# Kernel optimization log

Measured on AMD Instinct MI355X. Metric: run time of the kernel, lower is better.

## Reference

```python
import jax, jax.numpy as jnp
import numpy as np

B, T, D = 16, 512, 256          # batch, seq_len, d_model (= num features = num graph nodes N)
H, MC, K, DE, DH = 4, 4, 3, 10, 128
GS, SS, AS = 4, 6, 4            # global/sector/asset regime states
TAU = 0.5
STEPS = 3                       # diffusion steps
HID = max(64, D)
DEC_H = max(64, D // 2)


def setup_inputs() -> dict:
    key = jax.random.key(0)
    ks = iter(jax.random.split(key, 64))

    def nrm(shape, s=0.02):
        return (s * jax.random.normal(next(ks), shape)).astype(jnp.float32)

    z = lambda *s: jnp.zeros(s, jnp.float32)
    o = lambda *s: jnp.ones(s, jnp.float32)
    p = dict(
        x=jax.random.normal(next(ks), (B, T, D), dtype=jnp.float32),
        # hierarchical regime controller
        gW1=nrm((D, HID)), gb1=z(HID), g_ln_w=o(HID), g_ln_b=z(HID),
        gW2=nrm((HID, GS)), gb2=z(GS),
        sW1=nrm((D, HID)), sb1=z(HID), sW2=nrm((HID, D * SS)), sb2=z(D * SS),
        aW1=nrm((D, HID)), ab1=z(HID), aW2=nrm((HID, D * AS)), ab2=z(D * AS),
        global_prior=z(GS), sector_prior=z(SS), asset_prior=z(AS),
        g2f=nrm((GS, D)),
        sector_emb=jax.random.normal(next(ks), (SS, D), dtype=jnp.float32),
        asset_emb=jax.random.normal(next(ks), (AS, D), dtype=jnp.float32),
        # bidirectional temporal scan (BI-Mamba stand-in)
        decay_f=nrm((D,), 1.0), decay_b=nrm((D,), 1.0),
        tW=nrm((D, D)), tb=z(D),
        # Bayesian MAGAC + diffusion graph prior
        psi=nrm((H, D, DE), 0.1), log_sigma=jnp.full((H,), -2.0, jnp.float32),
        step_logits=jnp.linspace(-1.0, 0.5, STEPS).astype(jnp.float32),
        noise_scale=jnp.full((STEPS,), 0.05, jnp.float32),
        Wk=nrm((K + 1, T, DH)),
        mean_w=nrm((DH,)), mean_b=z(), lv_w=nrm((DH,)), lv_b=z(),
        # risk-aware decoder
        dW1=nrm((D, DEC_H)), db1=z(DEC_H), d_ln_w=o(DEC_H), d_ln_b=z(DEC_H),
        mW=nrm((DEC_H,)), mb=z(), lvW=nrm((DEC_H,)), lvb=z(),
        cW=nrm((DEC_H,)), cb=z(),
    )
    return p


def _ln(h, w, b):
    m = h.mean(-1, keepdims=True)
    v = h.var(-1, keepdims=True)  # biased, matches torch LayerNorm
    return (h - m) / jnp.sqrt(v + 1e-5) * w + b


def _gelu(h):
    return jax.nn.gelu(h, approximate=False)


def _gumbel_softmax(k, logits):
    u = jax.random.uniform(k, logits.shape, minval=1e-6, maxval=1.0 - 1e-6)
    g = -jnp.log(-jnp.log(u))
    return jax.nn.softmax((logits + g) / TAU, axis=-1)


def _fwd(x, gW1, gb1, g_ln_w, g_ln_b, gW2, gb2, sW1, sb1, sW2, sb2,
         aW1, ab1, aW2, ab2, global_prior, sector_prior, asset_prior,
         g2f, sector_emb, asset_emb, decay_f, decay_b, tW, tb,
         psi, log_sigma, step_logits, noise_scale, Wk,
         mean_w, mean_b, lv_w, lv_b,
         dW1, db1, d_ln_w, d_ln_b, mW, mb, lvW, lvb, cW, cb):
    rk = jax.random.key(42)
    k_g, k_s, k_a, k_eps, k_diff = jax.random.split(rk, 5)

    # ---- hierarchical regime controller ----
    seq_mean = x.mean(1)                               # (B, D)
    diff_summary = (x[:, 1:] - x[:, :-1]).mean(1)      # (B, D)
    g_logits = _gelu(_ln(seq_mean @ gW1 + gb1, g_ln_w, g_ln_b)) @ gW2 + gb2
    s_logits = (_gelu(seq_mean @ sW1 + sb1) @ sW2 + sb2).reshape(B, D, SS)
    a_logits = (_gelu(diff_summary @ aW1 + ab1) @ aW2 + ab2).reshape(B, D, AS)
    g_probs = _gumbel_softmax(k_g, g_logits)
    s_probs = _gumbel_softmax(k_s, s_logits)
    a_probs = _gumbel_softmax(k_a, a_logits)
    global_gate = g_probs @ g2f                                   # (B, D)
    # diagonal of einsum('bfs,sd->bfd') == einsum('bfs,sf->bf')
    sector_gate = jnp.einsum('bfs,sf->bf', s_probs, sector_emb)
    asset_gate = jnp.einsum('bfs,sf->bf', a_probs, asset_emb)
    feature_gate = jax.nn.sigmoid(global_gate + sector_gate + asset_gate)
    gated_x = x * feature_gate[:, None, :]

    # ---- bidirectional temporal EMA scan (BI-Mamba stand-in) ----
    af = jax.nn.sigmoid(decay_f)
    abk = jax.nn.sigmoid(decay_b)
    xs = gated_x.transpose(1, 0, 2)                    # (T, B, D)

    def ema(a):
        def step(h, xt):
            h = a * h + (1.0 - a) * xt
            return h, h
        return step

    _, hf = jax.lax.scan(ema(af), jnp.zeros_like(xs[0]), xs)
    _, hb = jax.lax.scan(ema(abk), jnp.zeros_like(xs[0]), xs[::-1])
    temporal = (hf + hb[::-1]).transpose(1, 0, 2) @ tW + tb       # (B, T, D)
    node_major = temporal.transpose(0, 2, 1)                      # (B, N=D, T)

    # ---- Bayesian adjacency sampling (MC samples per head) ----
    logits = jnp.einsum('hne,hme->hnm', psi, psi) / jnp.sqrt(jnp.float32(DE))
    sigma = jnp.exp(log_sigma)                                    # (H,)
    eps = jax.random.normal(k_eps, (MC, H, D, D))
    A = jax.nn.softmax(logits[None] + sigma[None, :, None, None] * eps, axis=-1)

    # ---- diffusion refinement guided by regime features ----
    ctx = feature_gate.mean(0)
    ctx = ctx / (jnp.linalg.norm(ctx) + 1e-6)
    outer = ctx[:, None] * ctx[None, :]
    outer = outer / jnp.maximum(outer.sum(-1, keepdims=True), 1e-6)
    dkeys = jax.random.split(k_diff, STEPS)
    for s in range(STEPS):                             # fixed small loop, vectorized over (MC,H)
        alpha = jax.nn.sigmoid(step_logits[s])
        noise = noise_scale[s] * jax.random.normal(dkeys[s], A.shape)
        A = alpha * A + (1.0 - alpha) * outer + noise
        A = 0.5 * (A + jnp.swapaxes(A, -1, -2))
        A = jax.nn.softmax(A, axis=-1)

    # ---- K-hop graph conv, averaged over MC samples and heads ----
    Z = jnp.einsum('bnt,td->bnd', node_major, Wk[0])[None, None]  # hop 0
    P = jnp.broadcast_to(node_major, (MC, H, B, D, T))
    for k in range(1, K + 1):
        P = jnp.einsum('mhnp,mhbpt->mhbnt', A, P)
        Z = Z + jnp.einsum('mhbnt,td->mhbnd', P, Wk[k])
    Z = Z.mean((0, 1))                                            # (B, N, DH)
    graph_mean = Z @ mean_w + mean_b                              # (B, N)
    graph_logvar = Z @ lv_w + lv_b                                # (B, N)

    # ---- risk-aware decoder ----
    feat = _ln(_gelu(graph_mean @ dW1 + db1), d_ln_w, d_ln_b)     # (B, DEC_H)
    mean = feat @ mW + mb
    dec_logvar = feat @ lvW + lvb
    _cvar = jax.nn.sigmoid(feat @ cW + cb)  # auxiliary head (not in returned output)
    var = jnp.exp(dec_logvar) + jnp.exp(graph_logvar).sum(1)
    log_var = jnp.log(var)
    return jnp.stack([mean, log_var], axis=-1)                    # (B, 2)


def reference(x, gW1, gb1, g_ln_w, g_ln_b, gW2, gb2, sW1, sb1, sW2, sb2,
              aW1, ab1, aW2, ab2, global_prior, sector_prior, asset_prior,
              g2f, sector_emb, asset_emb, decay_f, decay_b, tW, tb,
              psi, log_sigma, step_logits, noise_scale, Wk,
              mean_w, mean_b, lv_w, lv_b,
              dW1, db1, d_ln_w, d_ln_b, mW, mb, lvW, lvb, cW, cb):
    return _fwd(x, gW1, gb1, g_ln_w, g_ln_b, gW2, gb2, sW1, sb1, sW2, sb2,
                aW1, ab1, aW2, ab2, global_prior, sector_prior, asset_prior,
                g2f, sector_emb, asset_emb, decay_f, decay_b, tW, tb,
                psi, log_sigma, step_logits, noise_scale, Wk,
                mean_w, mean_b, lv_w, lv_b,
                dW1, db1, d_ln_w, d_ln_b, mW, mb, lvW, lvb, cW, cb)
```

## Files before the change

kernel.cpp:

```cpp
#include <hip/hip_runtime.h>
#include <stdint.h>

#define PARTITIONABLE 1

namespace {

struct TFPair { uint32_t a, b; };

__host__ __device__ constexpr uint32_t rotl32(uint32_t x, int d) {
  return (x << d) | (x >> (32 - d));
}

__host__ __device__ constexpr TFPair tf2x32(uint32_t k0, uint32_t k1,
                                            uint32_t x0, uint32_t x1) {
  uint32_t k2 = k0 ^ k1 ^ 0x1BD11BDAu;
  x0 += k0; x1 += k1;
  x0 += x1; x1 = rotl32(x1, 13); x1 ^= x0;
  x0 += x1; x1 = rotl32(x1, 15); x1 ^= x0;
  x0 += x1; x1 = rotl32(x1, 26); x1 ^= x0;
  x0 += x1; x1 = rotl32(x1, 6);  x1 ^= x0;
  x0 += k1; x1 += k2 + 1u;
  x0 += x1; x1 = rotl32(x1, 17); x1 ^= x0;
  x0 += x1; x1 = rotl32(x1, 29); x1 ^= x0;
  x0 += x1; x1 = rotl32(x1, 16); x1 ^= x0;
  x0 += x1; x1 = rotl32(x1, 24); x1 ^= x0;
  x0 += k2; x1 += k0 + 2u;
  x0 += x1; x1 = rotl32(x1, 13); x1 ^= x0;
  x0 += x1; x1 = rotl32(x1, 15); x1 ^= x0;
  x0 += x1; x1 = rotl32(x1, 26); x1 ^= x0;
  x0 += x1; x1 = rotl32(x1, 6);  x1 ^= x0;
  x0 += k0; x1 += k1 + 3u;
  x0 += x1; x1 = rotl32(x1, 17); x1 ^= x0;
  x0 += x1; x1 = rotl32(x1, 29); x1 ^= x0;
  x0 += x1; x1 = rotl32(x1, 16); x1 ^= x0;
  x0 += x1; x1 = rotl32(x1, 24); x1 ^= x0;
  x0 += k1; x1 += k2 + 4u;
  x0 += x1; x1 = rotl32(x1, 13); x1 ^= x0;
  x0 += x1; x1 = rotl32(x1, 15); x1 ^= x0;
  x0 += x1; x1 = rotl32(x1, 26); x1 ^= x0;
  x0 += x1; x1 = rotl32(x1, 6);  x1 ^= x0;
  x0 += k2; x1 += k0 + 5u;
  return TFPair{x0, x1};
}

#if PARTITIONABLE
constexpr TFPair KG  = tf2x32(0u, 42u, 0u, 0u);
constexpr TFPair KS  = tf2x32(0u, 42u, 0u, 1u);
constexpr TFPair KA  = tf2x32(0u, 42u, 0u, 2u);
constexpr TFPair KE  = tf2x32(0u, 42u, 0u, 3u);
constexpr TFPair KD  = tf2x32(0u, 42u, 0u, 4u);
constexpr TFPair DK0 = tf2x32(KD.a, KD.b, 0u, 0u);
constexpr TFPair DK1 = tf2x32(KD.a, KD.b, 0u, 1u);
constexpr TFPair DK2 = tf2x32(KD.a, KD.b, 0u, 2u);
#else
constexpr TFPair SP0 = tf2x32(0u, 42u, 0u, 5u);
constexpr TFPair SP1 = tf2x32(0u, 42u, 1u, 6u);
constexpr TFPair SP2 = tf2x32(0u, 42u, 2u, 7u);
constexpr TFPair SP3 = tf2x32(0u, 42u, 3u, 8u);
constexpr TFPair SP4 = tf2x32(0u, 42u, 4u, 9u);
constexpr TFPair KG  = TFPair{SP0.a, SP1.a};
constexpr TFPair KS  = TFPair{SP2.a, SP3.a};
constexpr TFPair KA  = TFPair{SP4.a, SP0.b};
constexpr TFPair KE  = TFPair{SP1.b, SP2.b};
constexpr TFPair KD  = TFPair{SP3.b, SP4.b};
constexpr TFPair DP0 = tf2x32(KD.a, KD.b, 0u, 3u);
constexpr TFPair DP1 = tf2x32(KD.a, KD.b, 1u, 4u);
constexpr TFPair DP2 = tf2x32(KD.a, KD.b, 2u, 5u);
constexpr TFPair DK0 = TFPair{DP0.a, DP1.a};
constexpr TFPair DK1 = TFPair{DP2.a, DP0.b};
constexpr TFPair DK2 = TFPair{DP1.b, DP2.b};
#endif

__device__ __forceinline__ uint32_t rbits(uint32_t k0, uint32_t k1,
                                          uint32_t idx, uint32_t half) {
#if PARTITIONABLE
  TFPair t = tf2x32(k0, k1, 0u, idx);
  return t.a ^ t.b;
#else
  if (idx < half) return tf2x32(k0, k1, idx, idx + half).a;
  return tf2x32(k0, k1, idx - half, idx).b;
#endif
}

__device__ __forceinline__ float bits_to_u01(uint32_t bits) {
  return __uint_as_float((bits >> 9) | 0x3F800000u) - 1.0f;
}

__device__ __forceinline__ float gumbel_u(uint32_t k0, uint32_t k1,
                                          uint32_t idx, uint32_t half) {
  const float mn = 1e-6f;
  const float mx = 1.0f - 1e-6f;
  float f = bits_to_u01(rbits(k0, k1, idx, half));
  return fmaxf(mn, f * (mx - mn) + mn);
}

__device__ __forceinline__ float erfinv_f32(float x) {
  float w = -log1pf(-x * x);
  float p;
  if (w < 5.0f) {
    w -= 2.5f;
    p = 2.81022636e-08f;
    p = fmaf(p, w, 3.43273939e-07f);
    p = fmaf(p, w, -3.5233877e-06f);
    p = fmaf(p, w, -4.39150654e-06f);
    p = fmaf(p, w, 0.00021858087f);
    p = fmaf(p, w, -0.00125372503f);
    p = fmaf(p, w, -0.00417768164f);
    p = fmaf(p, w, 0.246640727f);
    p = fmaf(p, w, 1.50140941f);
  } else {
    w = sqrtf(w) - 3.0f;
    p = -0.000200214257f;
    p = fmaf(p, w, 0.000100950558f);
    p = fmaf(p, w, 0.00134934322f);
    p = fmaf(p, w, -0.00367342844f);
    p = fmaf(p, w, 0.00573950773f);
    p = fmaf(p, w, -0.0076224613f);
    p = fmaf(p, w, 0.00943887047f);
    p = fmaf(p, w, 1.00167406f);
    p = fmaf(p, w, 2.83297682f);
  }
  return p * x;
}

__device__ __forceinline__ float normal_from(uint32_t k0, uint32_t k1,
                                             uint32_t idx, uint32_t half) {
  const float lo = -0x1.fffffep-1f;
  float f = bits_to_u01(rbits(k0, k1, idx, half));
  float u = fmaxf(lo, f * 2.0f + lo);
  return 1.41421356237f * erfinv_f32(u);
}

__device__ __forceinline__ float gelu_f(float x) {
  return 0.5f * x * (1.0f + erff(x / 1.4142135623730951f));
}
__device__ __forceinline__ float sigmoid_f(float x) {
  return 1.0f / (1.0f + expf(-x));
}

__device__ __forceinline__ float wave_sum(float v) {
  #pragma unroll
  for (int m = 32; m > 0; m >>= 1) v += __shfl_xor(v, m);
  return v;
}
__device__ __forceinline__ float wave_max(float v) {
  #pragma unroll
  for (int m = 32; m > 0; m >>= 1) v = fmaxf(v, __shfl_xor(v, m));
  return v;
}
template <int NW>
__device__ __forceinline__ float blk_sum(float v, float* slots) {
  v = wave_sum(v);
  int wid = threadIdx.x >> 6;
  if ((threadIdx.x & 63) == 0) slots[wid] = v;
  __syncthreads();
  float r = slots[0];
  #pragma unroll
  for (int i = 1; i < NW; ++i) r += slots[i];
  return r;
}
template <int NW>
__device__ __forceinline__ float blk_max(float v, float* slots) {
  v = wave_max(v);
  int wid = threadIdx.x >> 6;
  if ((threadIdx.x & 63) == 0) slots[wid] = v;
  __syncthreads();
  float r = slots[0];
  #pragma unroll
  for (int i = 1; i < NW; ++i) r = fmaxf(r, slots[i]);
  return r;
}

struct Params {
  const float *x, *gW1, *gb1, *glnw, *glnb, *gW2, *gb2, *sW1, *sb1, *sW2, *sb2,
      *aW1, *ab1, *aW2, *ab2, *g2f, *semb, *aemb, *decay_f, *decay_b, *tW, *tb,
      *psi, *log_sigma, *step_logits, *noise_scale, *Wk, *mean_w, *mean_b,
      *lv_w, *lv_b, *dW1, *db1, *dlnw, *dlnb, *mW, *mb, *lvW, *lvb;
  float* out;
  float *fg, *ctx, *v, *sv, *u, *Pf, *Qf, *Pb, *Qb, *Lf, *Lb, *YH, *R1, *R2,
      *gm, *glv, *A, *A2, *At, *At2;
};


__device__ __forceinline__ void phase_hidgates(const Params& P, float* smem,
                                               int task, int tid) {
  float* seqm = smem;
  float* dif  = smem + 256;
  float* hgGs = smem + 512;
  float* hgSs = smem + 768;
  float* hgAs = smem + 1024;
  float* lvS  = smem + 1280;
  float* lvA  = smem + 1664;
  float* gsl  = smem + 1920;
  float* gvals= smem + 1936;
  float* gpv  = smem + 1940;
  float* s1   = smem + 1944;
  float* s2   = smem + 1948;
  int b = task >> 2, f0 = (task & 3) * 64;
  const float* xb = P.x + (size_t)b * 512 * 256 + tid;
  float s = 0.f;
  for (int tc = 0; tc < 16; ++tc) {
    float ps = 0.f;
    for (int i = 0; i < 32; ++i) ps += xb[(size_t)(tc * 32 + i) * 256];
    s += ps;
  }
  seqm[tid] = s / 512.0f;
  dif[tid] = (xb[(size_t)511 * 256] - xb[0]) / 511.0f;
  __syncthreads();
  float hG = P.gb1[tid], hS = P.sb1[tid], hA = P.ab1[tid];
  for (int d = 0; d < 256; ++d) {
    float sm = seqm[d], df = dif[d];
    hG = fmaf(sm, P.gW1[d * 256 + tid], hG);
    hS = fmaf(sm, P.sW1[d * 256 + tid], hS);
    hA = fmaf(df, P.aW1[d * 256 + tid], hA);
  }
  {
    float mean = blk_sum<4>(hG, s1) / 256.0f;
    float dv = hG - mean;
    float var = blk_sum<4>(dv * dv, s2) / 256.0f;
    hG = dv / sqrtf(var + 1e-5f) * P.glnw[tid] + P.glnb[tid];
  }
  hgGs[tid] = gelu_f(hG);
  hgSs[tid] = gelu_f(hS);
  hgAs[tid] = gelu_f(hA);
  __syncthreads();
  float lg[4];
  #pragma unroll
  for (int sx = 0; sx < 4; ++sx)
    lg[sx] = blk_sum<4>(hgGs[tid] * P.gW2[tid * 4 + sx], gsl + 4 * sx);
  if (tid < 4) {
    float u = gumbel_u(KG.a, KG.b, (uint32_t)(b * 4 + tid), 32u);
    float g = -logf(-logf(u));
    gvals[tid] = (lg[tid] + P.gb2[tid] + g) / 0.5f;
  }
  __syncthreads();
  if (tid < 4) {
    float mx = fmaxf(fmaxf(gvals[0], gvals[1]), fmaxf(gvals[2], gvals[3]));
    float sum = expf(gvals[0] - mx) + expf(gvals[1] - mx) +
                expf(gvals[2] - mx) + expf(gvals[3] - mx);
    gpv[tid] = expf(gvals[tid] - mx) / sum;
  }
  {
    int o = tid;
    int fl = o / 6, sx = o - fl * 6;
    int f = f0 + fl;
    const float* wp = P.sW2 + f * 6 + sx;
    float acc = P.sb2[f * 6 + sx];
    for (int d = 0; d < 256; ++d) acc = fmaf(hgSs[d], wp[(size_t)d * 1536], acc);
    float u = gumbel_u(KS.a, KS.b, (uint32_t)(b * 256 + f) * 6u + sx, 12288u);
    lvS[o] = (acc + (-logf(-logf(u)))) / 0.5f;
  }
  if (tid < 128) {
    int o = tid + 256;
    int fl = o / 6, sx = o - fl * 6;
    int f = f0 + fl;
    const float* wp = P.sW2 + f * 6 + sx;
    float acc = P.sb2[f * 6 + sx];
    for (int d = 0; d < 256; ++d) acc = fmaf(hgSs[d], wp[(size_t)d * 1536], acc);
    float u = gumbel_u(KS.a, KS.b, (uint32_t)(b * 256 + f) * 6u + sx, 12288u);
    lvS[o] = (acc + (-logf(-logf(u)))) / 0.5f;
  }
  {
    int fl = tid >> 2, sx = tid & 3;
    int f = f0 + fl;
    const float* wp = P.aW2 + f * 4 + sx;
    float acc = P.ab2[f * 4 + sx];
    for (int d = 0; d < 256; ++d) acc = fmaf(hgAs[d], wp[(size_t)d * 1024], acc);
    float u = gumbel_u(KA.a, KA.b, (uint32_t)(b * 256 + f) * 4u + sx, 8192u);
    lvA[tid] = (acc + (-logf(-logf(u)))) / 0.5f;
  }
  __syncthreads();
  if (tid < 64) {
    int f = f0 + tid;
    float v0 = lvS[tid * 6 + 0], v1 = lvS[tid * 6 + 1], v2 = lvS[tid * 6 + 2];
    float v3 = lvS[tid * 6 + 3], v4 = lvS[tid * 6 + 4], v5 = lvS[tid * 6 + 5];
    float mx = fmaxf(fmaxf(fmaxf(v0, v1), fmaxf(v2, v3)), fmaxf(v4, v5));
    float e0 = expf(v0 - mx), e1 = expf(v1 - mx), e2 = expf(v2 - mx);
    float e3 = expf(v3 - mx), e4 = expf(v4 - mx), e5 = expf(v5 - mx);
    float ssum = e0 + e1 + e2 + e3 + e4 + e5;
    float sg = (e0 / ssum) * P.semb[0 * 256 + f] + (e1 / ssum) * P.semb[1 * 256 + f] +
               (e2 / ssum) * P.semb[2 * 256 + f] + (e3 / ssum) * P.semb[3 * 256 + f] +
               (e4 / ssum) * P.semb[4 * 256 + f] + (e5 / ssum) * P.semb[5 * 256 + f];
    float a0 = lvA[tid * 4 + 0], a1 = lvA[tid * 4 + 1];
    float a2 = lvA[tid * 4 + 2], a3 = lvA[tid * 4 + 3];
    float amx = fmaxf(fmaxf(a0, a1), fmaxf(a2, a3));
    float x0 = expf(a0 - amx), x1 = expf(a1 - amx);
    float x2 = expf(a2 - amx), x3 = expf(a3 - amx);
    float asum = x0 + x1 + x2 + x3;
    float ag = (x0 / asum) * P.aemb[0 * 256 + f] + (x1 / asum) * P.aemb[1 * 256 + f] +
               (x2 / asum) * P.aemb[2 * 256 + f] + (x3 / asum) * P.aemb[3 * 256 + f];
    float gg = 0.f;
    #pragma unroll
    for (int sx = 0; sx < 4; ++sx) gg = fmaf(gpv[sx], P.g2f[sx * 256 + f], gg);
    P.fg[b * 256 + f] = sigmoid_f(gg + sg + ag);
  }
}

__device__ __forceinline__ void phase_vcompute(const Params& P, int bid2,
                                               int tid) {
  int j = bid2 >> 2, tg = bid2 & 3;
  const float* wp = (j & 1) ? P.lv_w : P.mean_w;
  const float* Wkk = P.Wk + (size_t)(j >> 1) * 65536;
  int wid = tid >> 6, lane = tid & 63;
  float w0 = wp[lane], w1 = wp[64 + lane];
  float svloc = 0.f;
  for (int i = 0; i < 32; ++i) {
    int t = tg * 128 + wid * 32 + i;
    const float* row = Wkk + (size_t)t * 128;
    float s = row[lane] * w0 + row[64 + lane] * w1;
    s = wave_sum(s);
    if (lane == 0) { P.v[j * 512 + t] = s; svloc += s; }
  }
  if (lane == 0) P.sv[j * 16 + tg * 4 + wid] = svloc;
}

__device__ __forceinline__ void phase_ainit_row(const Params& P, float* smem,
                                                int blk, int tid) {
  float* pn = smem;
  float* s1 = smem + 12;
  float* s2 = smem + 16;
  int mh = blk >> 8, h = mh & 3, n = blk & 255, p = tid;
  if (p < 10) pn[p] = P.psi[(size_t)(h * 256 + n) * 10 + p];
  __syncthreads();
  const float* pp = P.psi + (size_t)(h * 256 + p) * 10;
  float s = 0.f;
  #pragma unroll
  for (int e = 0; e < 10; ++e) s = fmaf(pn[e], pp[e], s);
  float logit = s / sqrtf(10.0f);
  uint32_t idx = (uint32_t)blk * 256u + (uint32_t)p;
  float eps = normal_from(KE.a, KE.b, idx, 524288u);
  float val = logit + expf(P.log_sigma[h]) * eps;
  float mx = blk_max<4>(val, s1);
  float e = expf(val - mx);
  float sum = blk_sum<4>(e, s2);
  P.A[(size_t)blk * 256 + p] = e / sum;
}

__device__ __forceinline__ void phase_ctx(const Params& P, float* smem,
                                          int tid) {
  float* s1 = smem;
  float* s2 = smem + 4;
  float c = 0.f;
  for (int b = 0; b < 16; ++b) c += P.fg[b * 256 + tid];
  c /= 16.0f;
  float ss = blk_sum<4>(c * c, s1);
  float cv = c / (sqrtf(ss) + 1e-6f);
  P.ctx[tid] = cv;
  float S = blk_sum<4>(cv, s2);
  if (tid == 0) P.ctx[256] = S;
}

__device__ __forceinline__ void phase_transA(const Params& P, float* smem,
                                             int blk, int tid) {
  float* tile = smem;
  int mh = blk >> 6;
  int tr = ((blk >> 3) & 7) * 32, tc = (blk & 7) * 32;
  const float* src = P.A + (size_t)mh * 65536;
  float* dst = P.At + (size_t)mh * 65536;
  int lr = tid >> 5, lc = tid & 31;
  #pragma unroll
  for (int p = 0; p < 4; ++p) {
    int r = p * 8 + lr;
    tile[r * 33 + lc] = src[(size_t)(tr + r) * 256 + tc + lc];
  }
  __syncthreads();
  #pragma unroll
  for (int p = 0; p < 4; ++p) {
    int r = p * 8 + lr;
    dst[(size_t)(tc + r) * 256 + tr + lc] = tile[lc * 33 + r];
  }
}

__device__ __forceinline__ void phase_scan1(const Params& P, float* smem,
                                            int ch, int tid) {
  float* vv = smem;
  int b = ch >> 4, c = ch & 15;
  int d = tid;
  vv[(d >> 5) * 32 + (d & 31)] = P.v[(d >> 5) * 512 + c * 32 + (d & 31)];
  __syncthreads();
  float g = P.fg[b * 256 + d];
  float af = sigmoid_f(P.decay_f[d]);
  float ab = sigmoid_f(P.decay_b[d]);
  float r_gx[32];
  const float* xp = P.x + ((size_t)b * 512 + c * 32) * 256 + d;
  #pragma unroll
  for (int i = 0; i < 32; ++i) r_gx[i] = xp[(size_t)i * 256] * g;
  float h = 0.f, pw = 1.f;
  float Pr[8], Q[8];
  #pragma unroll
  for (int j = 0; j < 8; ++j) { Pr[j] = 0.f; Q[j] = 0.f; }
  #pragma unroll
  for (int i = 0; i < 32; ++i) {
    h = fmaf(af, h, (1.0f - af) * r_gx[i]);
    pw *= af;
    #pragma unroll
    for (int j = 0; j < 8; ++j) {
      float vj = vv[j * 32 + i];
      Pr[j] = fmaf(h, vj, Pr[j]);
      Q[j] = fmaf(pw, vj, Q[j]);
    }
  }
  size_t base = ((size_t)(b * 16 + c) * 8) * 256 + d;
  #pragma unroll
  for (int j = 0; j < 8; ++j) {
    P.Pf[base + j * 256] = Pr[j];
    P.Qf[base + j * 256] = Q[j];
  }
  P.Lf[(b * 16 + c) * 256 + d] = h;
  h = 0.f; pw = 1.f;
  #pragma unroll
  for (int j = 0; j < 8; ++j) { Pr[j] = 0.f; Q[j] = 0.f; }
  #pragma unroll
  for (int i = 31; i >= 0; --i) {
    h = fmaf(ab, h, (1.0f - ab) * r_gx[i]);
    pw *= ab;
    #pragma unroll
    for (int j = 0; j < 8; ++j) {
      float vj = vv[j * 32 + i];
      Pr[j] = fmaf(h, vj, Pr[j]);
      Q[j] = fmaf(pw, vj, Q[j]);
    }
  }
  #pragma unroll
  for (int j = 0; j < 8; ++j) {
    P.Pb[base + j * 256] = Pr[j];
    P.Qb[base + j * 256] = Q[j];
  }
  P.Lb[(b * 16 + c) * 256 + d] = h;
}

__device__ __forceinline__ void phase_scan2(const Params& P, int blk, int tid) {
  int b = blk >> 3, j = blk & 7;
  int d = tid;
  float af = sigmoid_f(P.decay_f[d]);
  float ab = sigmoid_f(P.decay_b[d]);
  float af32 = af, ab32 = ab;
  #pragma unroll
  for (int q = 0; q < 5; ++q) { af32 *= af32; ab32 *= ab32; }
  float acc = 0.f, H = 0.f;
  for (int c = 0; c < 16; ++c) {
    size_t base = ((size_t)(b * 16 + c) * 8 + j) * 256 + d;
    acc += P.Pf[base] + H * P.Qf[base];
    H = P.Lf[(b * 16 + c) * 256 + d] + af32 * H;
  }
  H = 0.f;
  for (int c = 15; c >= 0; --c) {
    size_t base = ((size_t)(b * 16 + c) * 8 + j) * 256 + d;
    acc += P.Pb[base] + H * P.Qb[base];
    H = P.Lb[(b * 16 + c) * 256 + d] + ab32 * H;
  }
  P.u[(b * 8 + j) * 256 + d] = acc;
}

__device__ __forceinline__ void phase_ygemm(const Params& P, float* smem,
                                            int blk32, int tid) {
  float* As = smem;
  float* Bs = smem + 1056;
  float* svs = smem + 2112;
  int n0 = (blk32 & 7) * 32, m0 = (blk32 >> 3) * 32;
  int tx = tid & 31, ty = tid >> 5;
  if (tid < 8) {
    float ssv = 0.f;
    #pragma unroll
    for (int q = 0; q < 16; ++q) ssv += P.sv[tid * 16 + q];
    svs[tid] = ssv;
  }
  float acc[4] = {0.f, 0.f, 0.f, 0.f};
  for (int k0 = 0; k0 < 256; k0 += 32) {
    #pragma unroll
    for (int l = 0; l < 4; ++l) {
      int e = tid + l * 256, r = e >> 5, cc = e & 31;
      As[r * 33 + cc] = P.u[(size_t)(m0 + r) * 256 + k0 + cc];
      Bs[r * 33 + cc] = P.tW[(size_t)(k0 + r) * 256 + n0 + cc];
    }
    __syncthreads();
    #pragma unroll
    for (int kk = 0; kk < 32; ++kk) {
      float bv = Bs[kk * 33 + tx];
      #pragma unroll
      for (int i = 0; i < 4; ++i)
        acc[i] = fmaf(As[(ty + 8 * i) * 33 + kk], bv, acc[i]);
    }
    __syncthreads();
  }
  int n = n0 + tx;
  float tbn = P.tb[n];
  float mb0 = P.mean_b[0], lb0 = P.lv_b[0];
  #pragma unroll
  for (int i = 0; i < 4; ++i) {
    int row = m0 + ty + 8 * i;
    int b = row >> 3, j = row & 7;
    float val = acc[i] + tbn * svs[j];
    if (j == 0) P.gm[b * 256 + n] = val + mb0;
    else if (j == 1) P.glv[b * 256 + n] = val + lb0;
    else {
      int k = (j >> 1) - 1, proj = j & 1;
      P.YH[k * 8192 + n * 32 + b * 2 + proj] = val;
    }
  }
}

template <bool WRITE_T>
__device__ __forceinline__ void phase_mix_tile(const Params& P, float* smem,
                                               int sidx, const float* Ain,
                                               const float* AinT, float* Aout,
                                               float* AoutT, uint32_t dk0,
                                               uint32_t dk1, int blk, int tid) {
  float* vals = smem;
  float* slots = smem + 16 * 257;
  int mh = blk >> 4, r0 = (blk & 15) * 16;
  float alpha = sigmoid_f(P.step_logits[sidx]);
  float ns = P.noise_scale[sidx];
  float S = P.ctx[256];
  int c = tid;
  float cp = P.ctx[c];
  const size_t mbase = (size_t)mh * 65536;
  #pragma unroll
  for (int r = 0; r < 16; ++r) {
    int n = r0 + r;
    float cn = P.ctx[n];
    float o_np = (cn * cp) / fmaxf(cn * S, 1e-6f);
    float o_pn = (cp * cn) / fmaxf(cp * S, 1e-6f);
    uint32_t i_np = (uint32_t)(mh * 65536 + n * 256 + c);
    uint32_t i_pn = (uint32_t)(mh * 65536 + c * 256 + n);
    float a_np = Ain[mbase + (size_t)n * 256 + c];
    float a_pn = AinT[mbase + (size_t)n * 256 + c];
    float m_np = alpha * a_np + (1.0f - alpha) * o_np +
                 ns * normal_from(dk0, dk1, i_np, 524288u);
    float m_pn = alpha * a_pn + (1.0f - alpha) * o_pn +
                 ns * normal_from(dk0, dk1, i_pn, 524288u);
    vals[r * 257 + c] = 0.5f * (m_np + m_pn);
  }
  __syncthreads();
  #pragma unroll
  for (int r = 0; r < 16; ++r) {
    float val = vals[r * 257 + c];
    float mx = blk_max<4>(val, slots + r * 8);
    float e = expf(val - mx);
    float sum = blk_sum<4>(e, slots + r * 8 + 4);
    float o = e / sum;
    Aout[mbase + (size_t)(r0 + r) * 256 + c] = o;
    if (WRITE_T) vals[r * 257 + c] = o;
  }
  if (WRITE_T) {
    __syncthreads();
    float tmp[16];
    #pragma unroll
    for (int r = 0; r < 16; ++r) tmp[r] = vals[r * 257 + c];
    float4* dst = (float4*)(AoutT + mbase + (size_t)c * 256 + r0);
    dst[0] = make_float4(tmp[0], tmp[1], tmp[2], tmp[3]);
    dst[1] = make_float4(tmp[4], tmp[5], tmp[6], tmp[7]);
    dst[2] = make_float4(tmp[8], tmp[9], tmp[10], tmp[11]);
    dst[3] = make_float4(tmp[12], tmp[13], tmp[14], tmp[15]);
  }
}

__device__ __forceinline__ void phase_horner(const Params& P, float* smem,
                                             const float* A, const float* Rin,
                                             int sRin, const float* Yadd,
                                             float* Rout, int bid, int tid) {
  float* As = smem;
  float* Bs = smem + 1056;
  int nt = bid & 7, mh = bid >> 3;
  int n0 = nt * 32;
  int tx = tid & 31, ty = tid >> 5;
  float acc[4] = {0.f, 0.f, 0.f, 0.f};
  const float* Ab = A + (size_t)mh * 65536;
  const float* Rb = Rin + (size_t)mh * sRin;
  for (int k0 = 0; k0 < 256; k0 += 32) {
    #pragma unroll
    for (int l = 0; l < 4; ++l) {
      int e = tid + l * 256, r = e >> 5, cc = e & 31;
      As[r * 33 + cc] = Ab[(size_t)(n0 + r) * 256 + k0 + cc];
      Bs[r * 33 + cc] = Rb[(size_t)(k0 + r) * 32 + cc];
    }
    __syncthreads();
    #pragma unroll
    for (int kk = 0; kk < 32; ++kk) {
      float bv = Bs[kk * 33 + tx];
      #pragma unroll
      for (int i = 0; i < 4; ++i)
        acc[i] = fmaf(As[(ty + 8 * i) * 33 + kk], bv, acc[i]);
    }
    __syncthreads();
  }
  #pragma unroll
  for (int i = 0; i < 4; ++i) {
    int n = n0 + ty + 8 * i;
    float vv = acc[i];
    if (Yadd) vv += Yadd[n * 32 + tx];
    Rout[(size_t)mh * 8192 + (size_t)n * 32 + tx] = vv;
  }
}

__device__ __forceinline__ void phase_findec(const Params& P, float* smem,
                                             int bid, int tid) {
  float* gmv = smem;
  float* sl = smem + 256;
  int b = bid;
  float sm_ = 0.f, sl_ = 0.f;
  for (int mh = 0; mh < 16; ++mh) {
    sm_ += P.R1[(size_t)mh * 8192 + tid * 32 + b * 2];
    sl_ += P.R1[(size_t)mh * 8192 + tid * 32 + b * 2 + 1];
  }
  float gmn = P.gm[b * 256 + tid] + sm_ * (1.0f / 16.0f);
  float gln = P.glv[b * 256 + tid] + sl_ * (1.0f / 16.0f);
  gmv[tid] = gmn;
  float se = expf(gln);
  __syncthreads();
  float sumexp = blk_sum<4>(se, sl);
  float h = 0.f;
  if (tid < 128) {
    h = P.db1[tid];
    for (int n = 0; n < 256; ++n) h = fmaf(gmv[n], P.dW1[n * 128 + tid], h);
    h = gelu_f(h);
  }
  float mean = blk_sum<4>(tid < 128 ? h : 0.f, sl + 4) / 128.0f;
  float dv = (tid < 128) ? h - mean : 0.f;
  float var = blk_sum<4>(dv * dv, sl + 8) / 128.0f;
  float feat = (tid < 128) ? dv / sqrtf(var + 1e-5f) * P.dlnw[tid] + P.dlnb[tid]
                           : 0.f;
  float m_c = blk_sum<4>(tid < 128 ? feat * P.mW[tid] : 0.f, sl + 12) + P.mb[0];
  float lv_c = blk_sum<4>(tid < 128 ? feat * P.lvW[tid] : 0.f, sl + 16) + P.lvb[0];
  if (tid == 0) {
    P.out[b * 2 + 0] = m_c;
    P.out[b * 2 + 1] = logf(expf(lv_c) + sumexp);
  }
}


__global__ __launch_bounds__(256) void kA(Params P) {
  __shared__ float smem[1952];
  int bid = blockIdx.x, tid = threadIdx.x;
  if (bid < 64) phase_hidgates(P, smem, bid, tid);
  else if (bid < 96) phase_vcompute(P, bid - 64, tid);
  else phase_ainit_row(P, smem, bid - 96, tid);
}

__global__ __launch_bounds__(256) void kB(Params P) {
  __shared__ float smem[1056];
  int bid = blockIdx.x, tid = threadIdx.x;
  if (bid < 256) phase_scan1(P, smem, bid, tid);
  else if (bid == 256) phase_ctx(P, smem, tid);
  else phase_transA(P, smem, bid - 257, tid);
}

__global__ __launch_bounds__(256) void kM0(Params P) {
  __shared__ float smem[4240];
  int bid = blockIdx.x, tid = threadIdx.x;
  if (bid < 256)
    phase_mix_tile<true>(P, smem, 0, P.A, P.At, P.A2, P.At2, DK0.a, DK0.b, bid, tid);
  else
    phase_scan2(P, bid - 256, tid);
}

__global__ __launch_bounds__(256) void kM1(Params P) {
  __shared__ float smem[4240];
  int bid = blockIdx.x, tid = threadIdx.x;
  if (bid < 256)
    phase_mix_tile<true>(P, smem, 1, P.A2, P.At2, P.A, P.At, DK1.a, DK1.b, bid, tid);
  else
    phase_ygemm(P, smem, bid - 256, tid);
}

__global__ __launch_bounds__(256) void kM2(Params P) {
  __shared__ float smem[4240];
  phase_mix_tile<false>(P, smem, 2, P.A, P.At, P.A2, nullptr, DK2.a, DK2.b,
                        blockIdx.x, threadIdx.x);
}

__global__ __launch_bounds__(256) void kH1(Params P) {
  __shared__ float smem[2112];
  phase_horner(P, smem, P.A2, P.YH + 2 * 8192, 0, P.YH + 8192, P.R1,
               blockIdx.x, threadIdx.x);
}
__global__ __launch_bounds__(256) void kH2(Params P) {
  __shared__ float smem[2112];
  phase_horner(P, smem, P.A2, P.R1, 8192, P.YH, P.R2, blockIdx.x, threadIdx.x);
}
__global__ __launch_bounds__(256) void kH3(Params P) {
  __shared__ float smem[2112];
  phase_horner(P, smem, P.A2, P.R2, 8192, nullptr, P.R1, blockIdx.x,
               threadIdx.x);
}

__global__ __launch_bounds__(256) void kFin(Params P) {
  __shared__ float smem[276];
  phase_findec(P, smem, blockIdx.x, threadIdx.x);
}

constexpr size_t O_FG = 0;
constexpr size_t O_CTX = 4096;
constexpr size_t O_V = 4480;
constexpr size_t O_SV = 8576;
constexpr size_t O_U = 8704;
constexpr size_t O_PF = 41472;
constexpr size_t O_QF = 565760;
constexpr size_t O_PB = 1090048;
constexpr size_t O_QB = 1614336;
constexpr size_t O_LF = 2138624;
constexpr size_t O_LB = 2204160;
constexpr size_t O_YH = 2269696;
constexpr size_t O_R1 = 2294272;
constexpr size_t O_R2 = 2425344;
constexpr size_t O_GM = 2556416;
constexpr size_t O_GLV = 2560512;
constexpr size_t O_A = 2564608;
constexpr size_t O_A2 = 3613184;
constexpr size_t O_AT = 4661760;
constexpr size_t O_AT2 = 5710336;

}

extern "C" void kernel_launch(void* const* d_in, const int* in_sizes, int n_in,
                              void* d_out, int out_size, void* d_ws,
                              size_t ws_size, hipStream_t stream) {
  (void)in_sizes; (void)n_in; (void)out_size; (void)ws_size;
  float* w = (float*)d_ws;
  Params prm;
  prm.x = (const float*)d_in[0];
  prm.gW1 = (const float*)d_in[1];
  prm.gb1 = (const float*)d_in[2];
  prm.glnw = (const float*)d_in[3];
  prm.glnb = (const float*)d_in[4];
  prm.gW2 = (const float*)d_in[5];
  prm.gb2 = (const float*)d_in[6];
  prm.sW1 = (const float*)d_in[7];
  prm.sb1 = (const float*)d_in[8];
  prm.sW2 = (const float*)d_in[9];
  prm.sb2 = (const float*)d_in[10];
  prm.aW1 = (const float*)d_in[11];
  prm.ab1 = (const float*)d_in[12];
  prm.aW2 = (const float*)d_in[13];
  prm.ab2 = (const float*)d_in[14];
  prm.g2f = (const float*)d_in[18];
  prm.semb = (const float*)d_in[19];
  prm.aemb = (const float*)d_in[20];
  prm.decay_f = (const float*)d_in[21];
  prm.decay_b = (const float*)d_in[22];
  prm.tW = (const float*)d_in[23];
  prm.tb = (const float*)d_in[24];
  prm.psi = (const float*)d_in[25];
  prm.log_sigma = (const float*)d_in[26];
  prm.step_logits = (const float*)d_in[27];
  prm.noise_scale = (const float*)d_in[28];
  prm.Wk = (const float*)d_in[29];
  prm.mean_w = (const float*)d_in[30];
  prm.mean_b = (const float*)d_in[31];
  prm.lv_w = (const float*)d_in[32];
  prm.lv_b = (const float*)d_in[33];
  prm.dW1 = (const float*)d_in[34];
  prm.db1 = (const float*)d_in[35];
  prm.dlnw = (const float*)d_in[36];
  prm.dlnb = (const float*)d_in[37];
  prm.mW = (const float*)d_in[38];
  prm.mb = (const float*)d_in[39];
  prm.lvW = (const float*)d_in[40];
  prm.lvb = (const float*)d_in[41];
  prm.out = (float*)d_out;
  prm.fg = w + O_FG;
  prm.ctx = w + O_CTX;
  prm.v = w + O_V;
  prm.sv = w + O_SV;
  prm.u = w + O_U;
  prm.Pf = w + O_PF;
  prm.Qf = w + O_QF;
  prm.Pb = w + O_PB;
  prm.Qb = w + O_QB;
  prm.Lf = w + O_LF;
  prm.Lb = w + O_LB;
  prm.YH = w + O_YH;
  prm.R1 = w + O_R1;
  prm.R2 = w + O_R2;
  prm.gm = w + O_GM;
  prm.glv = w + O_GLV;
  prm.A = w + O_A;
  prm.A2 = w + O_A2;
  prm.At = w + O_AT;
  prm.At2 = w + O_AT2;

  kA<<<4192, 256, 0, stream>>>(prm);
  kB<<<1281, 256, 0, stream>>>(prm);
  kM0<<<384, 256, 0, stream>>>(prm);
  kM1<<<288, 256, 0, stream>>>(prm);
  kM2<<<256, 256, 0, stream>>>(prm);
  kH1<<<128, 256, 0, stream>>>(prm);
  kH2<<<128, 256, 0, stream>>>(prm);
  kH3<<<128, 256, 0, stream>>>(prm);
  kFin<<<16, 256, 0, stream>>>(prm);
}
```

Measured before the change: 358.0 us.

## Split sequence-sum prepass, shrink mix tiles, fuse three Horner hops into one kernel

Moves the per-batch sequence sum of x out of the 64-block hidden-gate phase into a 256-block partial-sum prepass. The gate phase then reads 16 partial sums instead of scanning all 512 timesteps. Phases are regrouped: transA moves into the gate kernel and ctx runs alongside scan1. Mix tiles drop from 16 rows to 4, giving 1024 blocks per step with less shared memory each. The three Horner GEMM kernels become a single kernel that keeps the 2-column R slice in shared memory across hops, which drops two launches and the R2 buffer but re-reads the A rows three times from global or cache.

```diff
diff --git a/kernel.cpp b/kernel.cpp
--- a/kernel.cpp
+++ b/kernel.cpp
@@ -177,10 +177,22 @@
       *psi, *log_sigma, *step_logits, *noise_scale, *Wk, *mean_w, *mean_b,
       *lv_w, *lv_b, *dW1, *db1, *dlnw, *dlnb, *mW, *mb, *lvW, *lvb;
   float* out;
-  float *fg, *ctx, *v, *sv, *u, *Pf, *Qf, *Pb, *Qb, *Lf, *Lb, *YH, *R1, *R2,
-      *gm, *glv, *A, *A2, *At, *At2;
+  float *ps, *ds, *fg, *ctx, *v, *sv, *u, *Pf, *Qf, *Pb, *Qb, *Lf, *Lb, *YH,
+      *R1, *gm, *glv, *A, *A2, *At, *At2;
 };
 
+
+__device__ __forceinline__ void phase_ps(const Params& P, int bid, int tid) {
+  int b = bid >> 4, tc = bid & 15;
+  const float* xp = P.x + ((size_t)b * 512 + tc * 32) * 256 + tid;
+  float s = 0.f;
+  for (int i = 0; i < 32; ++i) s += xp[(size_t)i * 256];
+  P.ps[(size_t)bid * 256 + tid] = s;
+  if (tc == 0) {
+    const float* xb = P.x + (size_t)b * 512 * 256 + tid;
+    P.ds[b * 256 + tid] = (xb[(size_t)511 * 256] - xb[0]) / 511.0f;
+  }
+}
 
 __device__ __forceinline__ void phase_hidgates(const Params& P, float* smem,
                                                int task, int tid) {
@@ -197,15 +209,11 @@
   float* s1   = smem + 1944;
   float* s2   = smem + 1948;
   int b = task >> 2, f0 = (task & 3) * 64;
-  const float* xb = P.x + (size_t)b * 512 * 256 + tid;
+  const float* psb = P.ps + (size_t)(b * 16) * 256 + tid;
   float s = 0.f;
-  for (int tc = 0; tc < 16; ++tc) {
-    float ps = 0.f;
-    for (int i = 0; i < 32; ++i) ps += xb[(size_t)(tc * 32 + i) * 256];
-    s += ps;
-  }
+  for (int tc = 0; tc < 16; ++tc) s += psb[(size_t)tc * 256];
   seqm[tid] = s / 512.0f;
-  dif[tid] = (xb[(size_t)511 * 256] - xb[0]) / 511.0f;
+  dif[tid] = P.ds[b * 256 + tid];
   __syncthreads();
   float hG = P.gb1[tid], hS = P.sb1[tid], hA = P.ab1[tid];
   for (int d = 0; d < 256; ++d) {
@@ -501,14 +509,14 @@
 }
 
 template <bool WRITE_T>
-__device__ __forceinline__ void phase_mix_tile(const Params& P, float* smem,
-                                               int sidx, const float* Ain,
-                                               const float* AinT, float* Aout,
-                                               float* AoutT, uint32_t dk0,
-                                               uint32_t dk1, int blk, int tid) {
+__device__ __forceinline__ void phase_mix4(const Params& P, float* smem,
+                                           int sidx, const float* Ain,
+                                           const float* AinT, float* Aout,
+                                           float* AoutT, uint32_t dk0,
+                                           uint32_t dk1, int blk, int tid) {
   float* vals = smem;
-  float* slots = smem + 16 * 257;
-  int mh = blk >> 4, r0 = (blk & 15) * 16;
+  float* slots = smem + 4 * 257;
+  int mh = blk >> 6, r0 = (blk & 63) * 4;
   float alpha = sigmoid_f(P.step_logits[sidx]);
   float ns = P.noise_scale[sidx];
   float S = P.ctx[256];
@@ -516,7 +524,7 @@
   float cp = P.ctx[c];
   const size_t mbase = (size_t)mh * 65536;
   #pragma unroll
-  for (int r = 0; r < 16; ++r) {
+  for (int r = 0; r < 4; ++r) {
     int n = r0 + r;
     float cn = P.ctx[n];
     float o_np = (cn * cp) / fmaxf(cn * S, 1e-6f);
@@ -533,7 +541,7 @@
   }
   __syncthreads();
   #pragma unroll
-  for (int r = 0; r < 16; ++r) {
+  for (int r = 0; r < 4; ++r) {
     float val = vals[r * 257 + c];
     float mx = blk_max<4>(val, slots + r * 8);
     float e = expf(val - mx);
@@ -544,52 +552,10 @@
   }
   if (WRITE_T) {
     __syncthreads();
-    float tmp[16];
-    #pragma unroll
-    for (int r = 0; r < 16; ++r) tmp[r] = vals[r * 257 + c];
+    float t0 = vals[0 * 257 + c], t1 = vals[1 * 257 + c];
+    float t2 = vals[2 * 257 + c], t3 = vals[3 * 257 + c];
     float4* dst = (float4*)(AoutT + mbase + (size_t)c * 256 + r0);
-    dst[0] = make_float4(tmp[0], tmp[1], tmp[2], tmp[3]);
-    dst[1] = make_float4(tmp[4], tmp[5], tmp[6], tmp[7]);
-    dst[2] = make_float4(tmp[8], tmp[9], tmp[10], tmp[11]);
-    dst[3] = make_float4(tmp[12], tmp[13], tmp[14], tmp[15]);
-  }
-}
-
-__device__ __forceinline__ void phase_horner(const Params& P, float* smem,
-                                             const float* A, const float* Rin,
-                                             int sRin, const float* Yadd,
-                                             float* Rout, int bid, int tid) {
-  float* As = smem;
-  float* Bs = smem + 1056;
-  int nt = bid & 7, mh = bid >> 3;
-  int n0 = nt * 32;
-  int tx = tid & 31, ty = tid >> 5;
-  float acc[4] = {0.f, 0.f, 0.f, 0.f};
-  const float* Ab = A + (size_t)mh * 65536;
-  const float* Rb = Rin + (size_t)mh * sRin;
-  for (int k0 = 0; k0 < 256; k0 += 32) {
-    #pragma unroll
-    for (int l = 0; l < 4; ++l) {
-      int e = tid + l * 256, r = e >> 5, cc = e & 31;
-      As[r * 33 + cc] = Ab[(size_t)(n0 + r) * 256 + k0 + cc];
-      Bs[r * 33 + cc] = Rb[(size_t)(k0 + r) * 32 + cc];
-    }
-    __syncthreads();
-    #pragma unroll
-    for (int kk = 0; kk < 32; ++kk) {
-      float bv = Bs[kk * 33 + tx];
-      #pragma unroll
-      for (int i = 0; i < 4; ++i)
-        acc[i] = fmaf(As[(ty + 8 * i) * 33 + kk], bv, acc[i]);
-    }
-    __syncthreads();
-  }
-  #pragma unroll
-  for (int i = 0; i < 4; ++i) {
-    int n = n0 + ty + 8 * i;
-    float vv = acc[i];
-    if (Yadd) vv += Yadd[n * 32 + tx];
-    Rout[(size_t)mh * 8192 + (size_t)n * 32 + tx] = vv;
+    dst[0] = make_float4(t0, t1, t2, t3);
   }
 }
 
@@ -629,59 +595,89 @@
 }
 
 
-__global__ __launch_bounds__(256) void kA(Params P) {
+__global__ __launch_bounds__(256) void kPre(Params P) {
+  __shared__ float smem[20];
+  int bid = blockIdx.x, tid = threadIdx.x;
+  if (bid < 256) phase_ps(P, bid, tid);
+  else if (bid < 288) phase_vcompute(P, bid - 256, tid);
+  else phase_ainit_row(P, smem, bid - 288, tid);
+}
+
+__global__ __launch_bounds__(256) void kGate(Params P) {
   __shared__ float smem[1952];
   int bid = blockIdx.x, tid = threadIdx.x;
   if (bid < 64) phase_hidgates(P, smem, bid, tid);
-  else if (bid < 96) phase_vcompute(P, bid - 64, tid);
-  else phase_ainit_row(P, smem, bid - 96, tid);
-}
-
-__global__ __launch_bounds__(256) void kB(Params P) {
-  __shared__ float smem[1056];
+  else phase_transA(P, smem, bid - 64, tid);
+}
+
+__global__ __launch_bounds__(256) void kScan(Params P) {
+  __shared__ float smem[256];
   int bid = blockIdx.x, tid = threadIdx.x;
   if (bid < 256) phase_scan1(P, smem, bid, tid);
-  else if (bid == 256) phase_ctx(P, smem, tid);
-  else phase_transA(P, smem, bid - 257, tid);
+  else phase_ctx(P, smem, tid);
 }
 
 __global__ __launch_bounds__(256) void kM0(Params P) {
-  __shared__ float smem[4240];
+  __shared__ float smem[1060];
   int bid = blockIdx.x, tid = threadIdx.x;
-  if (bid < 256)
-    phase_mix_tile<true>(P, smem, 0, P.A, P.At, P.A2, P.At2, DK0.a, DK0.b, bid, tid);
+  if (bid < 1024)
+    phase_mix4<true>(P, smem, 0, P.A, P.At, P.A2, P.At2, DK0.a, DK0.b, bid, tid);
   else
-    phase_scan2(P, bid - 256, tid);
+    phase_scan2(P, bid - 1024, tid);
 }
 
 __global__ __launch_bounds__(256) void kM1(Params P) {
-  __shared__ float smem[4240];
+  __shared__ float smem[2120];
   int bid = blockIdx.x, tid = threadIdx.x;
-  if (bid < 256)
-    phase_mix_tile<true>(P, smem, 1, P.A2, P.At2, P.A, P.At, DK1.a, DK1.b, bid, tid);
+  if (bid < 1024)
+    phase_mix4<true>(P, smem, 1, P.A2, P.At2, P.A, P.At, DK1.a, DK1.b, bid, tid);
   else
-    phase_ygemm(P, smem, bid - 256, tid);
+    phase_ygemm(P, smem, bid - 1024, tid);
 }
 
 __global__ __launch_bounds__(256) void kM2(Params P) {
-  __shared__ float smem[4240];
-  phase_mix_tile<false>(P, smem, 2, P.A, P.At, P.A2, nullptr, DK2.a, DK2.b,
-                        blockIdx.x, threadIdx.x);
-}
-
-__global__ __launch_bounds__(256) void kH1(Params P) {
-  __shared__ float smem[2112];
-  phase_horner(P, smem, P.A2, P.YH + 2 * 8192, 0, P.YH + 8192, P.R1,
-               blockIdx.x, threadIdx.x);
-}
-__global__ __launch_bounds__(256) void kH2(Params P) {
-  __shared__ float smem[2112];
-  phase_horner(P, smem, P.A2, P.R1, 8192, P.YH, P.R2, blockIdx.x, threadIdx.x);
-}
-__global__ __launch_bounds__(256) void kH3(Params P) {
-  __shared__ float smem[2112];
-  phase_horner(P, smem, P.A2, P.R2, 8192, nullptr, P.R1, blockIdx.x,
-               threadIdx.x);
+  __shared__ float smem[1060];
+  phase_mix4<false>(P, smem, 2, P.A, P.At, P.A2, nullptr, DK2.a, DK2.b,
+                    blockIdx.x, threadIdx.x);
+}
+
+__global__ __launch_bounds__(256) void kHor(Params P) {
+  __shared__ float Rc[512];
+  int bid = blockIdx.x, tid = threadIdx.x;
+  int mh = bid >> 4, c0 = (bid & 15) * 2;
+  const float* Ab = P.A2 + (size_t)mh * 65536;
+  const float4* Arow = (const float4*)(Ab + (size_t)tid * 256);
+  const float* Y2 = P.YH + 2 * 8192;
+  Rc[tid * 2 + 0] = Y2[tid * 32 + c0 + 0];
+  Rc[tid * 2 + 1] = Y2[tid * 32 + c0 + 1];
+  __syncthreads();
+  #pragma unroll
+  for (int hop = 0; hop < 3; ++hop) {
+    float acc0 = 0.f, acc1 = 0.f;
+    const float4* Rc4 = (const float4*)Rc;
+    for (int k4 = 0; k4 < 64; ++k4) {
+      float4 a = Arow[k4];
+      float4 r01 = Rc4[k4 * 2];
+      float4 r23 = Rc4[k4 * 2 + 1];
+      acc0 = fmaf(a.x, r01.x, acc0); acc1 = fmaf(a.x, r01.y, acc1);
+      acc0 = fmaf(a.y, r01.z, acc0); acc1 = fmaf(a.y, r01.w, acc1);
+      acc0 = fmaf(a.z, r23.x, acc0); acc1 = fmaf(a.z, r23.y, acc1);
+      acc0 = fmaf(a.w, r23.z, acc0); acc1 = fmaf(a.w, r23.w, acc1);
+    }
+    if (hop == 0) {
+      acc0 += P.YH[8192 + tid * 32 + c0 + 0];
+      acc1 += P.YH[8192 + tid * 32 + c0 + 1];
+    } else if (hop == 1) {
+      acc0 += P.YH[tid * 32 + c0 + 0];
+      acc1 += P.YH[tid * 32 + c0 + 1];
+    }
+    __syncthreads();
+    Rc[tid * 2 + 0] = acc0;
+    Rc[tid * 2 + 1] = acc1;
+    __syncthreads();
+  }
+  P.R1[(size_t)mh * 8192 + (size_t)tid * 32 + c0 + 0] = Rc[tid * 2 + 0];
+  P.R1[(size_t)mh * 8192 + (size_t)tid * 32 + c0 + 1] = Rc[tid * 2 + 1];
 }
 
 __global__ __launch_bounds__(256) void kFin(Params P) {
@@ -702,13 +698,14 @@
 constexpr size_t O_LB = 2204160;
 constexpr size_t O_YH = 2269696;
 constexpr size_t O_R1 = 2294272;
-constexpr size_t O_R2 = 2425344;
-constexpr size_t O_GM = 2556416;
-constexpr size_t O_GLV = 2560512;
-constexpr size_t O_A = 2564608;
-constexpr size_t O_A2 = 3613184;
-constexpr size_t O_AT = 4661760;
-constexpr size_t O_AT2 = 5710336;
+constexpr size_t O_GM = 2425344;
+constexpr size_t O_GLV = 2429440;
+constexpr size_t O_A = 2433536;
+constexpr size_t O_A2 = 3482112;
+constexpr size_t O_AT = 4530688;
+constexpr size_t O_AT2 = 5579264;
+constexpr size_t O_PS = 6627840;
+constexpr size_t O_DS = 6693376;
 
 }
 
@@ -771,21 +768,21 @@
   prm.Lb = w + O_LB;
   prm.YH = w + O_YH;
   prm.R1 = w + O_R1;
-  prm.R2 = w + O_R2;
   prm.gm = w + O_GM;
   prm.glv = w + O_GLV;
   prm.A = w + O_A;
   prm.A2 = w + O_A2;
   prm.At = w + O_AT;
   prm.At2 = w + O_AT2;
-
-  kA<<<4192, 256, 0, stream>>>(prm);
-  kB<<<1281, 256, 0, stream>>>(prm);
-  kM0<<<384, 256, 0, stream>>>(prm);
-  kM1<<<288, 256, 0, stream>>>(prm);
-  kM2<<<256, 256, 0, stream>>>(prm);
-  kH1<<<128, 256, 0, stream>>>(prm);
-  kH2<<<128, 256, 0, stream>>>(prm);
-  kH3<<<128, 256, 0, stream>>>(prm);
+  prm.ps = w + O_PS;
+  prm.ds = w + O_DS;
+
+  kPre<<<4384, 256, 0, stream>>>(prm);
+  kGate<<<1088, 256, 0, stream>>>(prm);
+  kScan<<<257, 256, 0, stream>>>(prm);
+  kM0<<<1152, 256, 0, stream>>>(prm);
+  kM1<<<1056, 256, 0, stream>>>(prm);
+  kM2<<<1024, 256, 0, stream>>>(prm);
+  kHor<<<256, 256, 0, stream>>>(prm);
   kFin<<<16, 256, 0, stream>>>(prm);
 }
```

New measurement: 310.9 us. 1.15x faster.
